# Optimization experiments

Hardware: AMD Instinct MI355X
Metric: run time of the kernel (lower is better)

Reference implementation:

```python
import jax, jax.numpy as jnp
import numpy as np

N_EMBED = 512


def setup_inputs() -> dict:
    key = jax.random.key(0)
    k1, k2 = jax.random.split(key)
    inp = jax.random.normal(k1, (32, 4096, 64), dtype=jnp.float32)
    embed = jax.random.normal(k2, (64, N_EMBED), dtype=jnp.float32)  # [dim, n_embed]
    return {"input": inp, "embed": embed}


def reference(input, embed):
    dim = embed.shape[0]
    n_embed = embed.shape[1]
    flatten = input.reshape(-1, dim)  # [N, dim]
    # squared euclidean distance (argmin identical to cdist's argmin)
    dist = (
        jnp.sum(flatten * flatten, axis=1, keepdims=True)
        - 2.0 * (flatten @ embed)
        + jnp.sum(embed * embed, axis=0)[None, :]
    )  # [N, n_embed]
    embed_ind_flat = jnp.argmin(dist, axis=1)  # [N]
    embed_ind = embed_ind_flat.reshape(input.shape[:-1])
    # codebook lookup: embedding table is embed.T -> [n_embed, dim]
    quantize = embed.T[embed_ind]  # [..., dim]
    # training accumulators (equivalent to one_hot sums via segment_sum)
    embed_onehot_sum = jnp.zeros((n_embed,), flatten.dtype).at[embed_ind_flat].add(1.0)
    embed_sum = jax.ops.segment_sum(flatten, embed_ind_flat, num_segments=n_embed).T  # [dim, n_embed]
    diff = jnp.mean((jax.lax.stop_gradient(quantize) - input) ** 2)
    quantize_st = input + jax.lax.stop_gradient(quantize - input)
    return (quantize_st, diff, embed_ind, embed_onehot_sum, embed_sum)
```

## Files before the change

kernel.cpp:

```cpp
#include <hip/hip_runtime.h>
#include <hip/hip_bf16.h>

#define NROWS   131072
#define DIM     64
#define NEMB    512
#define OUT_Q     0
#define OUT_DIFF  8388608
#define OUT_IND   8388609
#define OUT_OH    8519681
#define OUT_ES    8520193
#define WS_EN     0
#define WS_ET     512
#define WS_EB     33280
#define WS_JIDX   66048
#define WS_HIST   197120
#define WS_CURS   205312
#define WS_FBUCK  213504
#define WS_ACC    344576
#define WS_DPART  377344
#define WS_NFLAG  379392
#define WS_NEED   379408
#define NWAVE_FIN 2048
#define NCOPY     16
#define TIE_TAU   0.05f

typedef float  f32x4  __attribute__((ext_vector_type(4)));
typedef short  s16x8  __attribute__((ext_vector_type(8)));

__device__ __forceinline__ unsigned short f2bf(float f) {
  unsigned u = __float_as_uint(f);
  return (unsigned short)((u + 0x7FFFu + ((u >> 16) & 1u)) >> 16);
}
__device__ __forceinline__ float bf2f(unsigned short h) {
  return __uint_as_float(((unsigned)h) << 16);
}

__global__ __launch_bounds__(256) void vq_prep(const float* __restrict__ embed,
                                               float* __restrict__ ws,
                                               float* __restrict__ out, int mode) {
  const int tid = blockIdx.x * 256 + threadIdx.x;
  const int nth = gridDim.x * 256;
  for (int e = tid; e < NEMB * DIM; e += nth) {
    int j = e >> 6, d = e & 63;
    ws[WS_ET + e] = embed[d * NEMB + j];
  }
  for (int j = tid; j < NEMB; j += nth) {
    float s = 0.f;
    for (int d = 0; d < DIM; ++d) {
      float v = embed[d * NEMB + j];
      s = fmaf(v, v, s);
    }
    ws[WS_EN + j] = s;
  }
  if (mode == 2) {
    unsigned short* eb = reinterpret_cast<unsigned short*>(ws + WS_EB);
    for (int f = tid; f < NEMB * 128; f += nth) {
      int i  = f & 7;
      int nl = (f >> 3) & 15;
      int g  = (f >> 7) & 3;
      int c  = (f >> 9) & 3;
      int T  = f >> 11;
      int j  = T * 16 + nl;
      int d  = (c & 1) * 32 + g * 8 + i;
      float e = embed[d * NEMB + j];
      unsigned short eh = f2bf(e);
      unsigned short v  = (c < 2) ? eh : f2bf(e - bf2f(eh));
      eb[f] = v;
    }
    unsigned* hist = reinterpret_cast<unsigned*>(ws + WS_HIST);
    for (int k = tid; k < NEMB * NCOPY; k += nth) hist[k] = 0u;
    for (int e = tid; e < NEMB * DIM; e += nth) ws[WS_ACC + e] = 0.f;
    if (tid == 0) reinterpret_cast<unsigned*>(ws + WS_NFLAG)[0] = 0u;
  } else {
    if (tid == 0) out[OUT_DIFF] = 0.f;
    for (int e = tid; e < NEMB + NEMB * DIM; e += nth) out[OUT_OH + e] = 0.f;
  }
}

#define MFMA16(A, B, C) __builtin_amdgcn_mfma_f32_16x16x32_bf16((A), (B), (C), 0, 0, 0)

__global__ __launch_bounds__(256) void vq_distm(
    const float* __restrict__ input, const float* __restrict__ ws,
    unsigned* __restrict__ jidx, unsigned* __restrict__ nflag,
    unsigned* __restrict__ flist) {
  __shared__ float en_lds[NEMB];
  const int tid  = threadIdx.x;
  const int lane = tid & 63;
  const int wid  = tid >> 6;
  const int nl   = lane & 15;
  const int g    = lane >> 4;
  en_lds[tid]       = ws[WS_EN + tid];
  en_lds[tid + 256] = ws[WS_EN + tid + 256];

  const int rowBase = blockIdx.x * 128 + wid * 32;

  s16x8 ah0_0, al0_0, ah1_0, al1_0;
  s16x8 ah0_1, al0_1, ah1_1, al1_1;
#define CVT1(V, H, L, O) { float _v = (V); unsigned _u = __float_as_uint(_v); \
    unsigned _r = (_u + 0x7FFFu + ((_u >> 16) & 1u)) >> 16; \
    float _hf = __uint_as_float(_r << 16); float _lf = _v - _hf; \
    unsigned _ul = __float_as_uint(_lf); \
    H[O] = (short)(unsigned short)_r; \
    L[O] = (short)(unsigned short)((_ul + 0x7FFFu + ((_ul >> 16) & 1u)) >> 16); }
#define CVT4(V, H, L, O) CVT1((V).x, H, L, (O)+0) CVT1((V).y, H, L, (O)+1) \
                         CVT1((V).z, H, L, (O)+2) CVT1((V).w, H, L, (O)+3)
  {
    const float* p0 = input + (size_t)(rowBase + nl) * DIM + g * 8;
    float4 a0 = *reinterpret_cast<const float4*>(p0);
    float4 a1 = *reinterpret_cast<const float4*>(p0 + 4);
    float4 b0 = *reinterpret_cast<const float4*>(p0 + 32);
    float4 b1 = *reinterpret_cast<const float4*>(p0 + 36);
    CVT4(a0, ah0_0, al0_0, 0) CVT4(a1, ah0_0, al0_0, 4)
    CVT4(b0, ah1_0, al1_0, 0) CVT4(b1, ah1_0, al1_0, 4)
    const float* p1 = input + (size_t)(rowBase + 16 + nl) * DIM + g * 8;
    float4 c0 = *reinterpret_cast<const float4*>(p1);
    float4 c1 = *reinterpret_cast<const float4*>(p1 + 4);
    float4 d0 = *reinterpret_cast<const float4*>(p1 + 32);
    float4 d1 = *reinterpret_cast<const float4*>(p1 + 36);
    CVT4(c0, ah0_1, al0_1, 0) CVT4(c1, ah0_1, al0_1, 4)
    CVT4(d0, ah1_1, al1_1, 0) CVT4(d1, ah1_1, al1_1, 4)
  }
  __syncthreads();

  float bD0[4], bD1[4], b2D0[4], b2D1[4]; int bJ0[4], bJ1[4];
#pragma unroll
  for (int r = 0; r < 4; ++r) {
    bD0[r] = 3.4e38f; bD1[r] = 3.4e38f; b2D0[r] = 3.4e38f; b2D1[r] = 3.4e38f;
    bJ0[r] = 0; bJ1[r] = 0;
  }

  const char* ebp = reinterpret_cast<const char*>(ws + WS_EB) + (size_t)lane * 16;
#pragma unroll 1
  for (int T = 0; T < 32; ++T) {
    const char* bt = ebp + (size_t)T * 4096;
    s16x8 B0 = *reinterpret_cast<const s16x8*>(bt);
    s16x8 B1 = *reinterpret_cast<const s16x8*>(bt + 1024);
    s16x8 B2 = *reinterpret_cast<const s16x8*>(bt + 2048);
    s16x8 B3 = *reinterpret_cast<const s16x8*>(bt + 3072);
    f32x4 aE0 = {0.f, 0.f, 0.f, 0.f}, aO0 = {0.f, 0.f, 0.f, 0.f};
    f32x4 aE1 = {0.f, 0.f, 0.f, 0.f}, aO1 = {0.f, 0.f, 0.f, 0.f};
    aE0 = MFMA16(ah0_0, B0, aE0); aE1 = MFMA16(ah0_1, B0, aE1);
    aO0 = MFMA16(ah1_0, B1, aO0); aO1 = MFMA16(ah1_1, B1, aO1);
    aE0 = MFMA16(al0_0, B0, aE0); aE1 = MFMA16(al0_1, B0, aE1);
    aO0 = MFMA16(al1_0, B1, aO0); aO1 = MFMA16(al1_1, B1, aO1);
    aE0 = MFMA16(ah0_0, B2, aE0); aE1 = MFMA16(ah0_1, B2, aE1);
    aO0 = MFMA16(ah1_0, B3, aO0); aO1 = MFMA16(ah1_1, B3, aO1);

    const float en0 = en_lds[(T << 4) | nl];
    const int jj = (T << 4) | nl;
#pragma unroll
    for (int r = 0; r < 4; ++r) {
      float d0 = fmaf(-2.0f, aE0[r] + aO0[r], en0);
      float d1 = fmaf(-2.0f, aE1[r] + aO1[r], en0);
      if (d0 < bD0[r]) { b2D0[r] = bD0[r]; bD0[r] = d0; bJ0[r] = jj; }
      else if (d0 < b2D0[r]) { b2D0[r] = d0; }
      if (d1 < bD1[r]) { b2D1[r] = bD1[r]; bD1[r] = d1; bJ1[r] = jj; }
      else if (d1 < b2D1[r]) { b2D1[r] = d1; }
    }
  }

#pragma unroll
  for (int r = 0; r < 4; ++r) {
#pragma unroll
    for (int t = 0; t < 2; ++t) {
      float D   = t ? bD1[r]  : bD0[r];
      float D2l = t ? b2D1[r] : b2D0[r];
      int   J   = t ? bJ1[r]  : bJ0[r];
      float Dm = D; int Jm = J;
#pragma unroll
      for (int s = 1; s <= 8; s <<= 1) {
        float oD = __shfl_xor(Dm, s, 64);
        int   oJ = __shfl_xor(Jm, s, 64);
        if (oD < Dm || (oD == Dm && oJ < Jm)) { Dm = oD; Jm = oJ; }
      }
      float cand = (D == Dm && J == Jm) ? D2l : D;
#pragma unroll
      for (int s = 1; s <= 8; s <<= 1) {
        float oc = __shfl_xor(cand, s, 64);
        if (oc < cand) cand = oc;
      }
      if (nl == 0) {
        int row = rowBase + t * 16 + g * 4 + r;
        jidx[row] = (unsigned)Jm;
        if (cand - Dm < TIE_TAU) {
          unsigned pos = atomicAdd(nflag, 1u);
          flist[pos] = (unsigned)row;
        }
      }
    }
  }
}

__global__ __launch_bounds__(256) void vq_refine(
    const float* __restrict__ input, const float* __restrict__ embed,
    const float* __restrict__ ws, const unsigned* __restrict__ nflag,
    const unsigned* __restrict__ flist, unsigned* __restrict__ jidx) {
  __shared__ float xl[DIM];
  __shared__ float rD[256];
  __shared__ int   rJ[256];
  const int tid = threadIdx.x;
  const unsigned n = nflag[0];

  for (unsigned t = blockIdx.x; t < n; t += gridDim.x) {
    const unsigned row = flist[t];
    if (tid < DIM) xl[tid] = input[(size_t)row * DIM + tid];
    __syncthreads();

    float xx = 0.f;
#pragma unroll
    for (int d = 0; d < DIM; ++d) xx = fmaf(xl[d], xl[d], xx);

    float best = 3.4e38f; int bj = tid;
#pragma unroll
    for (int h = 0; h < 2; ++h) {
      const int j = (h << 8) + tid;
      float acc = 0.f;
#pragma unroll
      for (int d = 0; d < DIM; ++d)
        acc = fmaf(xl[d], embed[d * NEMB + j], acc);
      float dist = (xx - 2.0f * acc) + ws[WS_EN + j];
      if (dist < best) { best = dist; bj = j; }
    }
    rD[tid] = best; rJ[tid] = bj;
    __syncthreads();
#pragma unroll
    for (int s = 128; s > 0; s >>= 1) {
      if (tid < s) {
        float oD = rD[tid + s]; int oJ = rJ[tid + s];
        if (oD < rD[tid] || (oD == rD[tid] && oJ < rJ[tid])) {
          rD[tid] = oD; rJ[tid] = oJ;
        }
      }
      __syncthreads();
    }
    if (tid == 0) jidx[row] = (unsigned)rJ[0];
    __syncthreads();
  }
}

__global__ __launch_bounds__(256) void vq_hist(
    const unsigned* __restrict__ jidx, unsigned* __restrict__ hist) {
  __shared__ unsigned lh[NEMB * NCOPY];
  const int tid = threadIdx.x;
  for (int k = tid; k < NEMB * NCOPY; k += 256) lh[k] = 0u;
  __syncthreads();
  for (int i = blockIdx.x * 256 + tid; i < NROWS; i += gridDim.x * 256)
    atomicAdd(&lh[(jidx[i] << 4) + ((i >> 8) & (NCOPY - 1))], 1u);
  __syncthreads();
  for (int k = tid; k < NEMB * NCOPY; k += 256)
    if (lh[k]) atomicAdd(hist + k, lh[k]);
}

__global__ __launch_bounds__(512) void vq_scan(
    const unsigned* __restrict__ hist, unsigned* __restrict__ curs,
    float* __restrict__ out) {
  __shared__ unsigned lsum[8];
  const int tid = threadIdx.x, lane = tid & 63, wid = tid >> 6;
  unsigned h[NCOPY];
  unsigned tot = 0;
#pragma unroll
  for (int p = 0; p < NCOPY; ++p) { h[p] = hist[(tid << 4) + p]; tot += h[p]; }
  unsigned v = tot;
#pragma unroll
  for (int s = 1; s < 64; s <<= 1) {
    unsigned t = (unsigned)__shfl_up((int)v, s, 64);
    if (lane >= s) v += t;
  }
  if (lane == 63) lsum[wid] = v;
  __syncthreads();
  if (tid == 0) {
    unsigned run = 0;
#pragma unroll
    for (int w = 0; w < 8; ++w) { unsigned t = lsum[w]; lsum[w] = run; run += t; }
  }
  __syncthreads();
  unsigned run = v - tot + lsum[wid];
#pragma unroll
  for (int p = 0; p < NCOPY; ++p) { curs[p * NEMB + tid] = run; run += h[p]; }
  out[OUT_OH + tid] = (float)tot;
}

__global__ __launch_bounds__(256) void vq_scatter(
    const unsigned* __restrict__ jidx, unsigned* __restrict__ curs,
    unsigned* __restrict__ bucket) {
  const int i = blockIdx.x * 256 + threadIdx.x;
  const unsigned J = jidx[i];
  const unsigned pos =
      atomicAdd(curs + (unsigned)(blockIdx.x & (NCOPY - 1)) * NEMB + J, 1u);
  bucket[pos] = (unsigned)i;
}

__global__ __launch_bounds__(256) void vq_finsum2(
    const float* __restrict__ input, const float* __restrict__ ws,
    const unsigned* __restrict__ jidx, const unsigned* __restrict__ bucket,
    float* __restrict__ ws_acc, float* __restrict__ dpart,
    float* __restrict__ out) {
  const int tid  = threadIdx.x;
  const int lane = tid & 63;
  const int wid  = tid >> 6;
  const int waveIdx = blockIdx.x * 4 + wid;
  const unsigned posBase = (unsigned)waveIdx * 64;

  float sum = 0.f, dacc = 0.f, q = 0.f;
  int jcur = -1;
  unsigned row = bucket[posBase];
  int j = (int)jidx[row];
#pragma unroll 1
  for (int p = 0; p < 64; ++p) {
    unsigned rowN = 0; int jN = 0;
    if (p < 63) {
      rowN = bucket[posBase + p + 1];
      jN = (int)jidx[rowN];
    }
    if (j != jcur) {
      if (jcur >= 0) atomicAdd(ws_acc + (size_t)jcur * DIM + lane, sum);
      sum = 0.f; jcur = j;
      q = ws[WS_ET + (size_t)j * DIM + lane];
    }
    const float xv = input[(size_t)row * DIM + lane];
    sum += xv;
    const float er = q - xv;
    dacc = fmaf(er, er, dacc);
    out[OUT_Q + (size_t)row * DIM + lane] = q;
    if (lane == 0) out[OUT_IND + row] = (float)j;
    row = rowN; j = jN;
  }
  atomicAdd(ws_acc + (size_t)jcur * DIM + lane, sum);
#pragma unroll
  for (int s = 1; s < 64; s <<= 1) dacc += __shfl_xor(dacc, s, 64);
  if (lane == 0) dpart[waveIdx] = dacc;
}

__global__ __launch_bounds__(256) void vq_es(
    const float* __restrict__ ws_acc, const float* __restrict__ dpart,
    float* __restrict__ out, int ndpart) {
  const int e = blockIdx.x * 256 + threadIdx.x;
  const int d = e >> 9, j = e & 511;
  out[OUT_ES + e] = ws_acc[(size_t)j * DIM + d];
  if (blockIdx.x == 0) {
    __shared__ float red[256];
    const int tid = threadIdx.x;
    float sum = 0.f;
    for (int k = tid; k < ndpart; k += 256) sum += dpart[k];
    red[tid] = sum;
    __syncthreads();
#pragma unroll
    for (int t = 128; t > 0; t >>= 1) {
      if (tid < t) red[tid] += red[tid + t];
      __syncthreads();
    }
    if (tid == 0) out[OUT_DIFF] = red[0] * (1.0f / (float)(NROWS * DIM));
  }
}

__global__ __launch_bounds__(256) void vq_mono(
    const float* __restrict__ input, const float* __restrict__ embed,
    const float* __restrict__ ws, float* __restrict__ out) {
  const int i = blockIdx.x * 256 + threadIdx.x;
  float x[DIM];
  const float4* xin = reinterpret_cast<const float4*>(input + (size_t)i * DIM);
#pragma unroll
  for (int k = 0; k < 16; ++k) {
    float4 v = xin[k];
    x[4 * k + 0] = v.x; x[4 * k + 1] = v.y; x[4 * k + 2] = v.z; x[4 * k + 3] = v.w;
  }
  float xx = 0.f;
#pragma unroll
  for (int d = 0; d < DIM; ++d) xx = fmaf(x[d], x[d], xx);
  float best = 3.4e38f; int bj = 0;
#pragma unroll 1
  for (int jt = 0; jt < NEMB; jt += 8) {
    float acc[8];
#pragma unroll
    for (int u = 0; u < 8; ++u) acc[u] = 0.f;
#pragma unroll
    for (int d = 0; d < DIM; ++d) {
      const float xv = x[d];
#pragma unroll
      for (int u = 0; u < 8; ++u)
        acc[u] = fmaf(xv, embed[d * NEMB + jt + u], acc[u]);
    }
#pragma unroll
    for (int u = 0; u < 8; ++u) {
      float dist = (xx - 2.0f * acc[u]) + ws[WS_EN + jt + u];
      if (dist < best) { best = dist; bj = jt + u; }
    }
  }
  out[OUT_IND + i] = (float)bj;
  const float4* qr = reinterpret_cast<const float4*>(ws + WS_ET + (size_t)bj * DIM);
  float4* qo = reinterpret_cast<float4*>(out + (size_t)i * DIM);
  float dsum = 0.f;
#pragma unroll
  for (int k = 0; k < 16; ++k) {
    float4 q = qr[k];
    float e0 = q.x - x[4 * k + 0]; dsum = fmaf(e0, e0, dsum);
    float e1 = q.y - x[4 * k + 1]; dsum = fmaf(e1, e1, dsum);
    float e2 = q.z - x[4 * k + 2]; dsum = fmaf(e2, e2, dsum);
    float e3 = q.w - x[4 * k + 3]; dsum = fmaf(e3, e3, dsum);
    qo[k] = q;
  }
  __shared__ float red[256];
  red[threadIdx.x] = dsum;
  __syncthreads();
#pragma unroll
  for (int s = 128; s > 0; s >>= 1) {
    if (threadIdx.x < s) red[threadIdx.x] += red[threadIdx.x + s];
    __syncthreads();
  }
  if (threadIdx.x == 0)
    atomicAdd(out + OUT_DIFF, red[0] * (1.0f / (float)(NROWS * DIM)));
  atomicAdd(out + OUT_OH + bj, 1.0f);
#pragma unroll
  for (int d = 0; d < DIM; ++d) atomicAdd(out + OUT_ES + d * NEMB + bj, x[d]);
}

extern "C" void kernel_launch(void* const* d_in, const int* in_sizes, int n_in,
                              void* d_out, int out_size, void* d_ws, size_t ws_size,
                              hipStream_t stream) {
  const float* input = (const float*)d_in[0];
  const float* embed = (const float*)d_in[1];
  float* out = (float*)d_out;
  float* ws  = (float*)d_ws;

  long ws_floats = (long)(ws_size / 4);

  if (ws_floats >= WS_NEED) {
    unsigned* jidx   = reinterpret_cast<unsigned*>(ws + WS_JIDX);
    unsigned* hist   = reinterpret_cast<unsigned*>(ws + WS_HIST);
    unsigned* curs   = reinterpret_cast<unsigned*>(ws + WS_CURS);
    unsigned* fbuck  = reinterpret_cast<unsigned*>(ws + WS_FBUCK);
    float*    ws_acc = ws + WS_ACC;
    float*    dpart  = ws + WS_DPART;
    unsigned* nflag  = reinterpret_cast<unsigned*>(ws + WS_NFLAG);
    vq_prep<<<256, 256, 0, stream>>>(embed, ws, out, 2);
    vq_distm<<<NROWS / 128, 256, 0, stream>>>(input, ws, jidx, nflag, fbuck);
    vq_refine<<<512, 256, 0, stream>>>(input, embed, ws, nflag, fbuck, jidx);
    vq_hist<<<128, 256, 0, stream>>>(jidx, hist);
    vq_scan<<<1, 512, 0, stream>>>(hist, curs, out);
    vq_scatter<<<NROWS / 256, 256, 0, stream>>>(jidx, curs, fbuck);
    vq_finsum2<<<NWAVE_FIN / 4, 256, 0, stream>>>(input, ws, jidx, fbuck,
                                                  ws_acc, dpart, out);
    vq_es<<<NEMB * DIM / 256, 256, 0, stream>>>(ws_acc, dpart, out, NWAVE_FIN);
  } else {
    vq_prep<<<256, 256, 0, stream>>>(embed, ws, out, 0);
    vq_mono<<<NROWS / 256, 256, 0, stream>>>(input, embed, ws, out);
  }
}
```

Measured before the change: 150.3 us.

## Fold histogram into distance/refine kernels and halve finsum rows per wave

Removes the separate vq_hist kernel by having vq_distm atomically increment the per-copy histogram as it writes each index, with vq_refine correcting counts when it changes an assignment. This drops one kernel launch and one full pass over jidx. Separately, finsum2 now processes 32 rows per wave with twice as many waves (NWAVE_FIN 4096, dpart region grown), aiming for more parallelism in the gather/accumulate stage. The trade-off is more global atomics in distm instead of LDS-aggregated ones, plus more partial-sum atomics into ws_acc.

```diff
diff --git a/kernel.cpp b/kernel.cpp
--- a/kernel.cpp
+++ b/kernel.cpp
@@ -18,9 +18,9 @@
 #define WS_FBUCK  213504
 #define WS_ACC    344576
 #define WS_DPART  377344
-#define WS_NFLAG  379392
-#define WS_NEED   379408
-#define NWAVE_FIN 2048
+#define WS_NFLAG  381440
+#define WS_NEED   381456
+#define NWAVE_FIN 4096
 #define NCOPY     16
 #define TIE_TAU   0.05f
 
@@ -82,7 +82,7 @@
 __global__ __launch_bounds__(256) void vq_distm(
     const float* __restrict__ input, const float* __restrict__ ws,
     unsigned* __restrict__ jidx, unsigned* __restrict__ nflag,
-    unsigned* __restrict__ flist) {
+    unsigned* __restrict__ flist, unsigned* __restrict__ hist) {
   __shared__ float en_lds[NEMB];
   const int tid  = threadIdx.x;
   const int lane = tid & 63;
@@ -182,6 +182,7 @@
       if (nl == 0) {
         int row = rowBase + t * 16 + g * 4 + r;
         jidx[row] = (unsigned)Jm;
+        atomicAdd(hist + (((unsigned)Jm) << 4) + ((unsigned)(row >> 8) & (NCOPY - 1)), 1u);
         if (cand - Dm < TIE_TAU) {
           unsigned pos = atomicAdd(nflag, 1u);
           flist[pos] = (unsigned)row;
@@ -194,7 +195,8 @@
 __global__ __launch_bounds__(256) void vq_refine(
     const float* __restrict__ input, const float* __restrict__ embed,
     const float* __restrict__ ws, const unsigned* __restrict__ nflag,
-    const unsigned* __restrict__ flist, unsigned* __restrict__ jidx) {
+    const unsigned* __restrict__ flist, unsigned* __restrict__ jidx,
+    unsigned* __restrict__ hist) {
   __shared__ float xl[DIM];
   __shared__ float rD[256];
   __shared__ int   rJ[256];
@@ -233,22 +235,18 @@
       }
       __syncthreads();
     }
-    if (tid == 0) jidx[row] = (unsigned)rJ[0];
+    if (tid == 0) {
+      const unsigned newJ = (unsigned)rJ[0];
+      const unsigned oldJ = jidx[row];
+      if (newJ != oldJ) {
+        const unsigned p = (row >> 8) & (NCOPY - 1);
+        atomicSub(hist + (oldJ << 4) + p, 1u);
+        atomicAdd(hist + (newJ << 4) + p, 1u);
+        jidx[row] = newJ;
+      }
+    }
     __syncthreads();
   }
-}
-
-__global__ __launch_bounds__(256) void vq_hist(
-    const unsigned* __restrict__ jidx, unsigned* __restrict__ hist) {
-  __shared__ unsigned lh[NEMB * NCOPY];
-  const int tid = threadIdx.x;
-  for (int k = tid; k < NEMB * NCOPY; k += 256) lh[k] = 0u;
-  __syncthreads();
-  for (int i = blockIdx.x * 256 + tid; i < NROWS; i += gridDim.x * 256)
-    atomicAdd(&lh[(jidx[i] << 4) + ((i >> 8) & (NCOPY - 1))], 1u);
-  __syncthreads();
-  for (int k = tid; k < NEMB * NCOPY; k += 256)
-    if (lh[k]) atomicAdd(hist + k, lh[k]);
 }
 
 __global__ __launch_bounds__(512) void vq_scan(
@@ -299,16 +297,16 @@
   const int lane = tid & 63;
   const int wid  = tid >> 6;
   const int waveIdx = blockIdx.x * 4 + wid;
-  const unsigned posBase = (unsigned)waveIdx * 64;
+  const unsigned posBase = (unsigned)waveIdx * 32;
 
   float sum = 0.f, dacc = 0.f, q = 0.f;
   int jcur = -1;
   unsigned row = bucket[posBase];
   int j = (int)jidx[row];
 #pragma unroll 1
-  for (int p = 0; p < 64; ++p) {
+  for (int p = 0; p < 32; ++p) {
     unsigned rowN = 0; int jN = 0;
-    if (p < 63) {
+    if (p < 31) {
       rowN = bucket[posBase + p + 1];
       jN = (int)jidx[rowN];
     }
@@ -433,9 +431,8 @@
     float*    dpart  = ws + WS_DPART;
     unsigned* nflag  = reinterpret_cast<unsigned*>(ws + WS_NFLAG);
     vq_prep<<<256, 256, 0, stream>>>(embed, ws, out, 2);
-    vq_distm<<<NROWS / 128, 256, 0, stream>>>(input, ws, jidx, nflag, fbuck);
-    vq_refine<<<512, 256, 0, stream>>>(input, embed, ws, nflag, fbuck, jidx);
-    vq_hist<<<128, 256, 0, stream>>>(jidx, hist);
+    vq_distm<<<NROWS / 128, 256, 0, stream>>>(input, ws, jidx, nflag, fbuck, hist);
+    vq_refine<<<512, 256, 0, stream>>>(input, embed, ws, nflag, fbuck, jidx, hist);
     vq_scan<<<1, 512, 0, stream>>>(hist, curs, out);
     vq_scatter<<<NROWS / 256, 256, 0, stream>>>(jidx, curs, fbuck);
     vq_finsum2<<<NWAVE_FIN / 4, 256, 0, stream>>>(input, ws, jidx, fbuck,
```

New measurement: 191.3 us. +27.3%, slower.
